# Kernel tuning notes

Hardware: AMD Instinct MI355X
Metric: run time of the kernel (lower is better)

Reference implementation:

```python
import jax, jax.numpy as jnp
import numpy as np

UNITS = 128
D_FEAT = 128
B, N = 4, 4096
EDGE_PROB = 0.01  # avg in-degree ~ N * EDGE_PROB ~ 41


def setup_inputs() -> dict:
    key = jax.random.key(0)
    k1, k2, k3, k4 = jax.random.split(key, 4)
    x = jax.random.normal(k1, (B, N, D_FEAT), dtype=jnp.float32)
    # binary adjacency mask, as consumed by tf.where(adj)
    adj = (jax.random.uniform(k2, (B, N, N)) < EDGE_PROB).astype(jnp.float32)
    # Dense(units, use_bias=False) kernels: msg on concat(x_snd, x_rec) -> [2d, U];
    # node_update on concat(x, messages) -> [d+U, U]
    W_msg = (jax.random.normal(k3, (2 * D_FEAT, UNITS), dtype=jnp.float32)
             / np.sqrt(2 * D_FEAT).astype(np.float32))
    W_upd = (jax.random.normal(k4, (D_FEAT + UNITS, UNITS), dtype=jnp.float32)
             / np.sqrt(D_FEAT + UNITS).astype(np.float32))
    return {"x": x, "adj": adj, "W_msg": W_msg, "W_upd": W_upd}


def reference(x, adj, W_msg, W_upd):
    # Faithful to MPNN2.call: edges are (b, s, r) where adj[b, s, r] != 0.
    # message per edge = concat(x[b,s], x[b,r]) @ W_msg = x[b,s]@Ws + x[b,r]@Wr.
    # messages[b,r] = segment_mean over incoming edges. Since the receiver term
    # x[b,r]@Wr is identical for all edges into r, its mean is itself, and the
    # sender term's mean is (adj^T @ (x@Ws)) / in_degree. Empty segments -> 0
    # (tf.math.unsorted_segment_mean semantics). This avoids data-dependent
    # edge-list shapes and is jit-compatible.
    d = x.shape[-1]
    Ws, Wr = W_msg[:d], W_msg[d:]          # [d, U] each
    xs = x @ Ws                            # sender contribution  [B, N, U]
    xr = x @ Wr                            # receiver contribution [B, N, U]
    deg = jnp.einsum('bsr->br', adj)[..., None]          # in-degree [B, N, 1]
    snd_sum = jnp.einsum('bsr,bsu->bru', adj, xs)        # [B, N, U]
    messages = jnp.where(deg > 0,
                         snd_sum / jnp.maximum(deg, 1.0) + xr,
                         0.0)
    # node_update on concat(x, messages); activation=None, use_bias=False
    return jnp.concatenate([x, messages], axis=-1) @ W_upd
```

## Files before the change

### kernel.cpp

```cpp
#include <hip/hip_runtime.h>
#include <hip/hip_bf16.h>

#define BB 4
#define NN 4096
#define ROWS (BB*NN)
#define RT 128
#define SC 512
#define NCH (NN/SC)
#define CAPC 32
#define BSTRIDE (NCH*CAPC)

typedef __attribute__((ext_vector_type(8))) short short8;
typedef __attribute__((ext_vector_type(4))) float f32x4;

__device__ __forceinline__ float asf(unsigned int u) {
    union { unsigned int i; float f; } cv; cv.i = u; return cv.f;
}
__device__ __forceinline__ unsigned short f2bf(float f) {
    union { float f; unsigned int i; } cv; cv.f = f;
    unsigned int i = cv.i;
    return (unsigned short)((i + 0x7FFFu + ((i >> 16) & 1u)) >> 16);
}

__global__ __launch_bounds__(256) void scan_bucket(const float* __restrict__ adj,
                                                   int* __restrict__ cnt2,
                                                   int* __restrict__ bucket) {
    __shared__ int lcnt[RT];
    int bI = blockIdx.x;
    int rt = bI & 31;
    int ch = (bI >> 5) & 7;
    int b  = bI >> 8;
    int r0 = rt * RT;
    int s0 = ch * SC;
    int t  = threadIdx.x;
    if (t < RT) lcnt[t] = 0;
    __syncthreads();
    int cg = t & 31;
    int sl = t >> 5;
    const float* base = adj + ((size_t)b * NN + s0) * NN + r0 + cg * 4;
    for (int k = 0; k < SC / 32; ++k) {
        float4 v[4];
#pragma unroll
        for (int u = 0; u < 4; ++u)
            v[u] = *(const float4*)(base + (size_t)(k * 32 + u * 8 + sl) * NN);
#pragma unroll
        for (int u = 0; u < 4; ++u) {
            int s = s0 + k * 32 + u * 8 + sl;
            float vals[4] = {v[u].x, v[u].y, v[u].z, v[u].w};
#pragma unroll
            for (int j = 0; j < 4; ++j) {
                if (vals[j] != 0.0f) {
                    int col = cg * 4 + j;
                    int slot = atomicAdd(&lcnt[col], 1);
                    if (slot < CAPC)
                        bucket[(size_t)((b << 12) + r0 + col) * BSTRIDE + ch * CAPC + slot] = s;
                }
            }
        }
    }
    __syncthreads();
    if (t < RT) cnt2[(size_t)((b << 12) + r0 + t) * NCH + ch] = lcnt[t];
}

__global__ __launch_bounds__(128) void fold_weights(const float* __restrict__ Wmsg,
                                                    const float* __restrict__ Wupd,
                                                    unsigned short* __restrict__ WcatT) {
    __shared__ float ldsS[128], ldsR[128];
    int k = blockIdx.x, t = threadIdx.x;
    ldsS[t] = Wmsg[k * 128 + t];
    ldsR[t] = Wmsg[(128 + k) * 128 + t];
    __syncthreads();
    float a1 = 0.f, a2 = 0.f;
#pragma unroll 8
    for (int m = 0; m < 128; ++m) {
        float wu = Wupd[(128 + m) * 128 + t];
        a1 += ldsS[m] * wu;
        a2 += ldsR[m] * wu;
    }
    WcatT[(size_t)t * 128 + k]         = f2bf(Wupd[k * 128 + t]);
    WcatT[(size_t)(128 + t) * 128 + k] = f2bf(a2);
    WcatT[(size_t)(256 + t) * 128 + k] = f2bf(a1);
}

__global__ __launch_bounds__(256) void gemm_mfma(const float* __restrict__ X,
                                                 const unsigned short* __restrict__ WcatT,
                                                 float* __restrict__ TD,
                                                 unsigned short* __restrict__ YB) {
    __shared__ unsigned short Al[64][136];
    __shared__ unsigned short Bl[128][136];
    int t  = threadIdx.x;
    int m0 = blockIdx.x * 64;
    int nb = blockIdx.y;

    {
        int m = t >> 2, seg = t & 3;
        const float* src = X + (size_t)(m0 + m) * 128 + seg * 32;
#pragma unroll
        for (int i = 0; i < 8; ++i) {
            float4 v = *(const float4*)(src + i * 4);
            ushort4 p;
            p.x = f2bf(v.x); p.y = f2bf(v.y); p.z = f2bf(v.z); p.w = f2bf(v.w);
            *(ushort4*)&Al[m][seg * 32 + i * 4] = p;
        }
    }
    {
        int n = t >> 1, half = t & 1;
        const unsigned short* src = WcatT + (size_t)(nb * 128 + n) * 128 + half * 64;
#pragma unroll
        for (int i = 0; i < 8; ++i) {
            uint4 v = *(const uint4*)(src + i * 8);
            *(uint4*)&Bl[n][half * 64 + i * 8] = v;
        }
    }
    __syncthreads();

    int lane = t & 63, wave = t >> 6;
    int quad = lane >> 4, lr = lane & 15;
    int wm = wave * 16;
    f32x4 acc[8];
#pragma unroll
    for (int s = 0; s < 8; ++s) acc[s] = (f32x4)0.f;

#pragma unroll
    for (int kk = 0; kk < 4; ++kk) {
        short8 a = *(short8*)&Al[wm + lr][kk * 32 + quad * 8];
#pragma unroll
        for (int s = 0; s < 8; ++s) {
            short8 bf = *(short8*)&Bl[s * 16 + lr][kk * 32 + quad * 8];
            acc[s] = __builtin_amdgcn_mfma_f32_16x16x32_bf16(a, bf, acc[s], 0, 0, 0);
        }
    }

    if (nb == 2) {
#pragma unroll
        for (int s = 0; s < 8; ++s)
#pragma unroll
            for (int r = 0; r < 4; ++r) {
                int row = m0 + wm + quad * 4 + r;
                YB[(size_t)row * 128 + s * 16 + lr] = f2bf(acc[s][r]);
            }
    } else {
#pragma unroll
        for (int s = 0; s < 8; ++s)
#pragma unroll
            for (int r = 0; r < 4; ++r) {
                int row = m0 + wm + quad * 4 + r;
                TD[(size_t)row * 256 + nb * 128 + s * 16 + lr] = acc[s][r];
            }
    }
}

__global__ __launch_bounds__(256) void gather_out(const float* __restrict__ TD,
                                                  const unsigned int* __restrict__ YB,
                                                  const int* __restrict__ cnt2,
                                                  const int* __restrict__ bucket,
                                                  float* __restrict__ out) {
    __shared__ int lds_s[4][BSTRIDE];
    int t  = threadIdx.x;
    int rs = t >> 6;
    int j2 = t & 63;
    int rg = blockIdx.x * 4 + rs;

    int c[NCH];
    int ctot = 0, deg = 0;
    int pre[NCH];
#pragma unroll
    for (int ch = 0; ch < NCH; ++ch) {
        c[ch] = cnt2[(size_t)rg * NCH + ch];
        deg += c[ch];
        int cc = min(c[ch], CAPC);
        pre[ch] = ctot;
        ctot += cc;
    }
#pragma unroll
    for (int ch = 0; ch < NCH; ++ch) {
        int cc = min(c[ch], CAPC);
        if (j2 < cc)
            lds_s[rs][pre[ch] + j2] = bucket[(size_t)rg * BSTRIDE + ch * CAPC + j2];
    }
    __syncthreads();

    const float2* td = (const float2*)(TD + (size_t)rg * 256);
    float2 t1 = td[j2];
    float2 res = t1;
    if (deg > 0) {
        int b = rg >> 12;
        const unsigned int* yb = YB + (((size_t)b << 12)) * 64 + j2;
        float al0 = 0.f, ah0 = 0.f, al1 = 0.f, ah1 = 0.f;
        float al2 = 0.f, ah2 = 0.f, al3 = 0.f, ah3 = 0.f;
        int e = 0;
        for (; e + 4 <= ctot; e += 4) {
            int s0 = lds_s[rs][e + 0];
            int s1 = lds_s[rs][e + 1];
            int s2 = lds_s[rs][e + 2];
            int s3 = lds_s[rs][e + 3];
            unsigned u0 = yb[(size_t)s0 * 64];
            unsigned u1 = yb[(size_t)s1 * 64];
            unsigned u2 = yb[(size_t)s2 * 64];
            unsigned u3 = yb[(size_t)s3 * 64];
            al0 += asf(u0 << 16); ah0 += asf(u0 & 0xffff0000u);
            al1 += asf(u1 << 16); ah1 += asf(u1 & 0xffff0000u);
            al2 += asf(u2 << 16); ah2 += asf(u2 & 0xffff0000u);
            al3 += asf(u3 << 16); ah3 += asf(u3 & 0xffff0000u);
        }
        for (; e < ctot; ++e) {
            unsigned u = yb[(size_t)lds_s[rs][e] * 64];
            al0 += asf(u << 16); ah0 += asf(u & 0xffff0000u);
        }
        float inv = 1.0f / (float)deg;
        float2 d2 = td[64 + j2];
        res.x = t1.x + d2.x + (al0 + al1 + al2 + al3) * inv;
        res.y = t1.y + d2.y + (ah0 + ah1 + ah2 + ah3) * inv;
    }
    ((float2*)(out + (size_t)rg * 128))[j2] = res;
}

extern "C" void kernel_launch(void* const* d_in, const int* in_sizes, int n_in,
                              void* d_out, int out_size, void* d_ws, size_t ws_size,
                              hipStream_t stream) {
    const float* x    = (const float*)d_in[0];
    const float* adj  = (const float*)d_in[1];
    const float* Wmsg = (const float*)d_in[2];
    const float* Wupd = (const float*)d_in[3];
    float* out = (float*)d_out;

    char* ws = (char*)d_ws;
    unsigned short* WcatT  = (unsigned short*)(ws);
    float*          TD     = (float*)(ws + 131072);
    unsigned short* YB     = (unsigned short*)(ws + 131072 + 16777216);
    int*            cnt2   = (int*)(ws + 131072 + 16777216 + 4194304);
    int*            bucket = (int*)(ws + 131072 + 16777216 + 4194304 + 524288);

    scan_bucket<<<1024, 256, 0, stream>>>(adj, cnt2, bucket);
    fold_weights<<<128, 128, 0, stream>>>(Wmsg, Wupd, WcatT);
    gemm_mfma<<<dim3(256, 3), 256, 0, stream>>>(x, WcatT, TD, YB);
    gather_out<<<ROWS / 4, 256, 0, stream>>>(TD, (const unsigned int*)YB, cnt2, bucket, out);
}
```

Measured before the change: 430.1 us.

## Scan full adjacency rows per block with double-buffered loads and finer sender chunks

The adjacency scan now has each block cover 32 full sender rows across all 4096 receivers, so reads are fully contiguous per row, and it double-buffers the row loads to overlap memory with atomic bucket insertion. Sender chunks shrink to 32 with capacity 8 per chunk, giving 128 chunks per receiver. The gather kernel rebuilds per-receiver edge lists with wave-level prefix scans over the 128 chunk counts. The risks are fewer blocks (512) for a bandwidth-bound scan, a larger count array, and strided reads of counts in the gather.

```diff
diff --git a/kernel.cpp b/kernel.cpp
--- a/kernel.cpp
+++ b/kernel.cpp
@@ -4,10 +4,9 @@
 #define BB 4
 #define NN 4096
 #define ROWS (BB*NN)
-#define RT 128
-#define SC 512
+#define SC 32
 #define NCH (NN/SC)
-#define CAPC 32
+#define CAPC 8
 #define BSTRIDE (NCH*CAPC)
 
 typedef __attribute__((ext_vector_type(8))) short short8;
@@ -25,41 +24,53 @@
 __global__ __launch_bounds__(256) void scan_bucket(const float* __restrict__ adj,
                                                    int* __restrict__ cnt2,
                                                    int* __restrict__ bucket) {
-    __shared__ int lcnt[RT];
-    int bI = blockIdx.x;
-    int rt = bI & 31;
-    int ch = (bI >> 5) & 7;
-    int b  = bI >> 8;
-    int r0 = rt * RT;
+    __shared__ int lcnt[NN];
+    int t  = threadIdx.x;
+    int ch = blockIdx.x & (NCH - 1);
+    int b  = blockIdx.x >> 7;
     int s0 = ch * SC;
-    int t  = threadIdx.x;
-    if (t < RT) lcnt[t] = 0;
-    __syncthreads();
-    int cg = t & 31;
-    int sl = t >> 5;
-    const float* base = adj + ((size_t)b * NN + s0) * NN + r0 + cg * 4;
-    for (int k = 0; k < SC / 32; ++k) {
-        float4 v[4];
-#pragma unroll
-        for (int u = 0; u < 4; ++u)
-            v[u] = *(const float4*)(base + (size_t)(k * 32 + u * 8 + sl) * NN);
-#pragma unroll
-        for (int u = 0; u < 4; ++u) {
-            int s = s0 + k * 32 + u * 8 + sl;
-            float vals[4] = {v[u].x, v[u].y, v[u].z, v[u].w};
+#pragma unroll
+    for (int i = 0; i < NN / 256; ++i) lcnt[i * 256 + t] = 0;
+    __syncthreads();
+
+    const float* base = adj + ((size_t)b * NN + s0) * NN;
+
+    float4 va[4], vb[4];
+    auto LOADROW = [&](float4* V, int r) {
+        const float4* rp = (const float4*)(base + (size_t)r * NN) + t;
+#pragma unroll
+        for (int i = 0; i < 4; ++i) V[i] = rp[i * 256];
+    };
+    auto PROCROW = [&](float4* V, int r) {
+        int s = s0 + r;
+#pragma unroll
+        for (int i = 0; i < 4; ++i) {
+            float vals[4] = {V[i].x, V[i].y, V[i].z, V[i].w};
 #pragma unroll
             for (int j = 0; j < 4; ++j) {
                 if (vals[j] != 0.0f) {
-                    int col = cg * 4 + j;
+                    int col = ((i << 8) + t) * 4 + j;
                     int slot = atomicAdd(&lcnt[col], 1);
                     if (slot < CAPC)
-                        bucket[(size_t)((b << 12) + r0 + col) * BSTRIDE + ch * CAPC + slot] = s;
+                        bucket[((size_t)((b << 12) + col) << 10) + (ch << 3) + slot] = s;
                 }
             }
         }
-    }
-    __syncthreads();
-    if (t < RT) cnt2[(size_t)((b << 12) + r0 + t) * NCH + ch] = lcnt[t];
+    };
+
+    LOADROW(va, 0);
+    for (int r = 0; r < SC; r += 2) {
+        LOADROW(vb, r + 1);
+        PROCROW(va, r);
+        if (r + 2 < SC) LOADROW(va, r + 2);
+        PROCROW(vb, r + 1);
+    }
+    __syncthreads();
+#pragma unroll
+    for (int i = 0; i < NN / 256; ++i) {
+        int col = i * 256 + t;
+        cnt2[((size_t)((b << 7) + ch) << 12) + col] = lcnt[col];
+    }
 }
 
 __global__ __launch_bounds__(128) void fold_weights(const float* __restrict__ Wmsg,
@@ -158,34 +169,42 @@
     __shared__ int lds_s[4][BSTRIDE];
     int t  = threadIdx.x;
     int rs = t >> 6;
-    int j2 = t & 63;
+    int l  = t & 63;
     int rg = blockIdx.x * 4 + rs;
-
-    int c[NCH];
-    int ctot = 0, deg = 0;
-    int pre[NCH];
-#pragma unroll
-    for (int ch = 0; ch < NCH; ++ch) {
-        c[ch] = cnt2[(size_t)rg * NCH + ch];
-        deg += c[ch];
-        int cc = min(c[ch], CAPC);
-        pre[ch] = ctot;
-        ctot += cc;
-    }
-#pragma unroll
-    for (int ch = 0; ch < NCH; ++ch) {
-        int cc = min(c[ch], CAPC);
-        if (j2 < cc)
-            lds_s[rs][pre[ch] + j2] = bucket[(size_t)rg * BSTRIDE + ch * CAPC + j2];
-    }
+    int b  = rg >> 12;
+    int r  = rg & (NN - 1);
+
+    int c0 = cnt2[((size_t)((b << 7) + l) << 12) + r];
+    int c1 = cnt2[((size_t)((b << 7) + 64 + l) << 12) + r];
+    int cc0 = min(c0, CAPC), cc1 = min(c1, CAPC);
+
+    int dsum = c0 + c1;
+#pragma unroll
+    for (int d = 32; d; d >>= 1) dsum += __shfl_xor(dsum, d, 64);
+    int deg = dsum;
+
+    int i0 = cc0;
+#pragma unroll
+    for (int d = 1; d < 64; d <<= 1) { int y = __shfl_up(i0, d, 64); if (l >= d) i0 += y; }
+    int i1 = cc1;
+#pragma unroll
+    for (int d = 1; d < 64; d <<= 1) { int y = __shfl_up(i1, d, 64); if (l >= d) i1 += y; }
+    int tot0 = __shfl(i0, 63, 64);
+    int tot1 = __shfl(i1, 63, 64);
+    int ex0  = i0 - cc0;
+    int ex1  = tot0 + i1 - cc1;
+    int ctot = tot0 + tot1;
+
+    const int* brow = bucket + ((size_t)rg << 10);
+    for (int k = 0; k < cc0; ++k) lds_s[rs][ex0 + k] = brow[(l << 3) + k];
+    for (int k = 0; k < cc1; ++k) lds_s[rs][ex1 + k] = brow[((64 + l) << 3) + k];
     __syncthreads();
 
     const float2* td = (const float2*)(TD + (size_t)rg * 256);
-    float2 t1 = td[j2];
+    float2 t1 = td[l];
     float2 res = t1;
     if (deg > 0) {
-        int b = rg >> 12;
-        const unsigned int* yb = YB + (((size_t)b << 12)) * 64 + j2;
+        const unsigned int* yb = YB + ((size_t)b << 12) * 64 + l;
         float al0 = 0.f, ah0 = 0.f, al1 = 0.f, ah1 = 0.f;
         float al2 = 0.f, ah2 = 0.f, al3 = 0.f, ah3 = 0.f;
         int e = 0;
@@ -208,11 +227,11 @@
             al0 += asf(u << 16); ah0 += asf(u & 0xffff0000u);
         }
         float inv = 1.0f / (float)deg;
-        float2 d2 = td[64 + j2];
+        float2 d2 = td[64 + l];
         res.x = t1.x + d2.x + (al0 + al1 + al2 + al3) * inv;
         res.y = t1.y + d2.y + (ah0 + ah1 + ah2 + ah3) * inv;
     }
-    ((float2*)(out + (size_t)rg * 128))[j2] = res;
+    ((float2*)(out + (size_t)rg * 128))[l] = res;
 }
 
 extern "C" void kernel_launch(void* const* d_in, const int* in_sizes, int n_in,
@@ -229,9 +248,9 @@
     float*          TD     = (float*)(ws + 131072);
     unsigned short* YB     = (unsigned short*)(ws + 131072 + 16777216);
     int*            cnt2   = (int*)(ws + 131072 + 16777216 + 4194304);
-    int*            bucket = (int*)(ws + 131072 + 16777216 + 4194304 + 524288);
-
-    scan_bucket<<<1024, 256, 0, stream>>>(adj, cnt2, bucket);
+    int*            bucket = (int*)(ws + 131072 + 16777216 + 4194304 + 8388608);
+
+    scan_bucket<<<BB * NCH, 256, 0, stream>>>(adj, cnt2, bucket);
     fold_weights<<<128, 128, 0, stream>>>(Wmsg, Wupd, WcatT);
     gemm_mfma<<<dim3(256, 3), 256, 0, stream>>>(x, WcatT, TD, YB);
     gather_out<<<ROWS / 4, 256, 0, stream>>>(TD, (const unsigned int*)YB, cnt2, bucket, out);
```

After: 456.1 us. +6.0%, slower.

## Replace bucket scan and gather with dense MFMA SpMM over adjacency

Applied to the files above, without the earlier changes.

Drops the sparse edge-bucketing scan and per-edge gather. Instead, a dense bf16 MFMA GEMM multiplies adj^T by a transposed bf16 YB, with the in-degree accumulated while loading each adjacency tile. The gemm epilogue now writes YB transposed per batch so the B operand reads are contiguous. This removes the CAPC=32 per-chunk cap that could truncate neighbours. The cost is dense compute over the whole 256MB adjacency, which becomes strided column loads, plus bf16 rounding of adjacency values (exact for 0/1).

```diff
diff --git a/kernel.cpp b/kernel.cpp
--- a/kernel.cpp
+++ b/kernel.cpp
@@ -1,65 +1,16 @@
 #include <hip/hip_runtime.h>
-#include <hip/hip_bf16.h>
 
 #define BB 4
 #define NN 4096
 #define ROWS (BB*NN)
-#define RT 128
-#define SC 512
-#define NCH (NN/SC)
-#define CAPC 32
-#define BSTRIDE (NCH*CAPC)
 
 typedef __attribute__((ext_vector_type(8))) short short8;
 typedef __attribute__((ext_vector_type(4))) float f32x4;
 
-__device__ __forceinline__ float asf(unsigned int u) {
-    union { unsigned int i; float f; } cv; cv.i = u; return cv.f;
-}
 __device__ __forceinline__ unsigned short f2bf(float f) {
     union { float f; unsigned int i; } cv; cv.f = f;
     unsigned int i = cv.i;
     return (unsigned short)((i + 0x7FFFu + ((i >> 16) & 1u)) >> 16);
-}
-
-__global__ __launch_bounds__(256) void scan_bucket(const float* __restrict__ adj,
-                                                   int* __restrict__ cnt2,
-                                                   int* __restrict__ bucket) {
-    __shared__ int lcnt[RT];
-    int bI = blockIdx.x;
-    int rt = bI & 31;
-    int ch = (bI >> 5) & 7;
-    int b  = bI >> 8;
-    int r0 = rt * RT;
-    int s0 = ch * SC;
-    int t  = threadIdx.x;
-    if (t < RT) lcnt[t] = 0;
-    __syncthreads();
-    int cg = t & 31;
-    int sl = t >> 5;
-    const float* base = adj + ((size_t)b * NN + s0) * NN + r0 + cg * 4;
-    for (int k = 0; k < SC / 32; ++k) {
-        float4 v[4];
-#pragma unroll
-        for (int u = 0; u < 4; ++u)
-            v[u] = *(const float4*)(base + (size_t)(k * 32 + u * 8 + sl) * NN);
-#pragma unroll
-        for (int u = 0; u < 4; ++u) {
-            int s = s0 + k * 32 + u * 8 + sl;
-            float vals[4] = {v[u].x, v[u].y, v[u].z, v[u].w};
-#pragma unroll
-            for (int j = 0; j < 4; ++j) {
-                if (vals[j] != 0.0f) {
-                    int col = cg * 4 + j;
-                    int slot = atomicAdd(&lcnt[col], 1);
-                    if (slot < CAPC)
-                        bucket[(size_t)((b << 12) + r0 + col) * BSTRIDE + ch * CAPC + slot] = s;
-                }
-            }
-        }
-    }
-    __syncthreads();
-    if (t < RT) cnt2[(size_t)((b << 12) + r0 + t) * NCH + ch] = lcnt[t];
 }
 
 __global__ __launch_bounds__(128) void fold_weights(const float* __restrict__ Wmsg,
@@ -85,7 +36,7 @@
 __global__ __launch_bounds__(256) void gemm_mfma(const float* __restrict__ X,
                                                  const unsigned short* __restrict__ WcatT,
                                                  float* __restrict__ TD,
-                                                 unsigned short* __restrict__ YB) {
+                                                 unsigned short* __restrict__ YBT) {
     __shared__ unsigned short Al[64][136];
     __shared__ unsigned short Bl[128][136];
     int t  = threadIdx.x;
@@ -132,13 +83,16 @@
     }
 
     if (nb == 2) {
-#pragma unroll
-        for (int s = 0; s < 8; ++s)
-#pragma unroll
-            for (int r = 0; r < 4; ++r) {
-                int row = m0 + wm + quad * 4 + r;
-                YB[(size_t)row * 128 + s * 16 + lr] = f2bf(acc[s][r]);
-            }
+        int b = m0 >> 12;
+        int s_base = (m0 & (NN - 1)) + wm + quad * 4;
+#pragma unroll
+        for (int s = 0; s < 8; ++s) {
+            int n = s * 16 + lr;
+            ushort4 p;
+            p.x = f2bf(acc[s][0]); p.y = f2bf(acc[s][1]);
+            p.z = f2bf(acc[s][2]); p.w = f2bf(acc[s][3]);
+            *(ushort4*)&YBT[(((size_t)(b << 7) + n) << 12) + s_base] = p;
+        }
     } else {
 #pragma unroll
         for (int s = 0; s < 8; ++s)
@@ -150,69 +104,100 @@
     }
 }
 
-__global__ __launch_bounds__(256) void gather_out(const float* __restrict__ TD,
-                                                  const unsigned int* __restrict__ YB,
-                                                  const int* __restrict__ cnt2,
-                                                  const int* __restrict__ bucket,
-                                                  float* __restrict__ out) {
-    __shared__ int lds_s[4][BSTRIDE];
+#define RT 32
+#define KT 128
+#define NT (NN/KT)
+__global__ __launch_bounds__(256) void spmm_out(const float* __restrict__ adj,
+                                                const unsigned short* __restrict__ YBT,
+                                                const float* __restrict__ TD,
+                                                float* __restrict__ out) {
+    __shared__ unsigned short At[RT][KT + 8];
+    __shared__ float degp[8][RT];
+    __shared__ float deg_s[RT];
+
     int t  = threadIdx.x;
-    int rs = t >> 6;
-    int j2 = t & 63;
-    int rg = blockIdx.x * 4 + rs;
-
-    int c[NCH];
-    int ctot = 0, deg = 0;
-    int pre[NCH];
-#pragma unroll
-    for (int ch = 0; ch < NCH; ++ch) {
-        c[ch] = cnt2[(size_t)rg * NCH + ch];
-        deg += c[ch];
-        int cc = min(c[ch], CAPC);
-        pre[ch] = ctot;
-        ctot += cc;
-    }
-#pragma unroll
-    for (int ch = 0; ch < NCH; ++ch) {
-        int cc = min(c[ch], CAPC);
-        if (j2 < cc)
-            lds_s[rs][pre[ch] + j2] = bucket[(size_t)rg * BSTRIDE + ch * CAPC + j2];
-    }
-    __syncthreads();
-
-    const float2* td = (const float2*)(TD + (size_t)rg * 256);
-    float2 t1 = td[j2];
-    float2 res = t1;
-    if (deg > 0) {
-        int b = rg >> 12;
-        const unsigned int* yb = YB + (((size_t)b << 12)) * 64 + j2;
-        float al0 = 0.f, ah0 = 0.f, al1 = 0.f, ah1 = 0.f;
-        float al2 = 0.f, ah2 = 0.f, al3 = 0.f, ah3 = 0.f;
-        int e = 0;
-        for (; e + 4 <= ctot; e += 4) {
-            int s0 = lds_s[rs][e + 0];
-            int s1 = lds_s[rs][e + 1];
-            int s2 = lds_s[rs][e + 2];
-            int s3 = lds_s[rs][e + 3];
-            unsigned u0 = yb[(size_t)s0 * 64];
-            unsigned u1 = yb[(size_t)s1 * 64];
-            unsigned u2 = yb[(size_t)s2 * 64];
-            unsigned u3 = yb[(size_t)s3 * 64];
-            al0 += asf(u0 << 16); ah0 += asf(u0 & 0xffff0000u);
-            al1 += asf(u1 << 16); ah1 += asf(u1 & 0xffff0000u);
-            al2 += asf(u2 << 16); ah2 += asf(u2 & 0xffff0000u);
-            al3 += asf(u3 << 16); ah3 += asf(u3 & 0xffff0000u);
-        }
-        for (; e < ctot; ++e) {
-            unsigned u = yb[(size_t)lds_s[rs][e] * 64];
-            al0 += asf(u << 16); ah0 += asf(u & 0xffff0000u);
-        }
-        float inv = 1.0f / (float)deg;
-        float2 d2 = td[64 + j2];
-        res.x = t1.x + d2.x + (al0 + al1 + al2 + al3) * inv;
-        res.y = t1.y + d2.y + (ah0 + ah1 + ah2 + ah3) * inv;
-    }
-    ((float2*)(out + (size_t)rg * 128))[j2] = res;
+    int r0 = blockIdx.x * RT;
+    int b  = blockIdx.y;
+    const float* adj_b = adj + (size_t)b * NN * NN;
+
+    int r  = t & 31;
+    int kg = t >> 5;
+    float va[16];
+    float dpart = 0.f;
+
+    int lane = t & 63, wave = t >> 6;
+    int wr = wave & 1, wn = wave >> 1;
+    int quad = lane >> 4, lr = lane & 15;
+    const unsigned short* ybt = YBT + ((size_t)b << 19);
+
+    f32x4 acc0 = (f32x4)0.f, acc1 = (f32x4)0.f, acc2 = (f32x4)0.f, acc3 = (f32x4)0.f;
+
+    {
+        const float* p = adj_b + (size_t)(kg * 16) * NN + r0 + r;
+#pragma unroll
+        for (int j = 0; j < 16; ++j) va[j] = p[(size_t)j * NN];
+    }
+
+    for (int tt = 0; tt < NT; ++tt) {
+        __syncthreads();
+        short8 w0, w1;
+#pragma unroll
+        for (int j = 0; j < 8; ++j) {
+            w0[j] = (short)f2bf(va[j]);
+            w1[j] = (short)f2bf(va[j + 8]);
+            dpart += va[j] + va[j + 8];
+        }
+        *(short8*)&At[r][kg * 16]     = w0;
+        *(short8*)&At[r][kg * 16 + 8] = w1;
+        __syncthreads();
+        if (tt + 1 < NT) {
+            const float* p = adj_b + (size_t)((tt + 1) * KT + kg * 16) * NN + r0 + r;
+#pragma unroll
+            for (int j = 0; j < 16; ++j) va[j] = p[(size_t)j * NN];
+        }
+        int k0 = tt * KT;
+#pragma unroll
+        for (int kk = 0; kk < 4; ++kk) {
+            short8 a = *(short8*)&At[wr * 16 + lr][kk * 32 + quad * 8];
+            const unsigned short* bp = ybt + (((size_t)(wn * 64 + lr)) << 12) + k0 + kk * 32 + quad * 8;
+            short8 b0 = *(const short8*)(bp);
+            short8 b1 = *(const short8*)(bp + (16 << 12));
+            short8 b2 = *(const short8*)(bp + (32 << 12));
+            short8 b3 = *(const short8*)(bp + (48 << 12));
+            acc0 = __builtin_amdgcn_mfma_f32_16x16x32_bf16(a, b0, acc0, 0, 0, 0);
+            acc1 = __builtin_amdgcn_mfma_f32_16x16x32_bf16(a, b1, acc1, 0, 0, 0);
+            acc2 = __builtin_amdgcn_mfma_f32_16x16x32_bf16(a, b2, acc2, 0, 0, 0);
+            acc3 = __builtin_amdgcn_mfma_f32_16x16x32_bf16(a, b3, acc3, 0, 0, 0);
+        }
+    }
+
+    __syncthreads();
+    degp[kg][r] = dpart;
+    __syncthreads();
+    if (t < RT) {
+        float s = 0.f;
+#pragma unroll
+        for (int g = 0; g < 8; ++g) s += degp[g][t];
+        deg_s[t] = s;
+    }
+    __syncthreads();
+
+    const float* td = TD + ((size_t)(b * NN + r0)) * 256;
+    float* ob = out + ((size_t)(b * NN + r0)) * 128;
+#pragma unroll
+    for (int sf = 0; sf < 4; ++sf) {
+        f32x4 a = (sf == 0) ? acc0 : (sf == 1) ? acc1 : (sf == 2) ? acc2 : acc3;
+        int n = wn * 64 + sf * 16 + lr;
+#pragma unroll
+        for (int rr = 0; rr < 4; ++rr) {
+            int rl = wr * 16 + quad * 4 + rr;
+            float deg = deg_s[rl];
+            float v = td[(size_t)rl * 256 + n];
+            if (deg > 0.f)
+                v += td[(size_t)rl * 256 + 128 + n] + a[rr] / deg;
+            ob[(size_t)rl * 128 + n] = v;
+        }
+    }
 }
 
 extern "C" void kernel_launch(void* const* d_in, const int* in_sizes, int n_in,
@@ -225,14 +210,11 @@
     float* out = (float*)d_out;
 
     char* ws = (char*)d_ws;
-    unsigned short* WcatT  = (unsigned short*)(ws);
-    float*          TD     = (float*)(ws + 131072);
-    unsigned short* YB     = (unsigned short*)(ws + 131072 + 16777216);
-    int*            cnt2   = (int*)(ws + 131072 + 16777216 + 4194304);
-    int*            bucket = (int*)(ws + 131072 + 16777216 + 4194304 + 524288);
-
-    scan_bucket<<<1024, 256, 0, stream>>>(adj, cnt2, bucket);
+    unsigned short* WcatT = (unsigned short*)(ws);
+    float*          TD    = (float*)(ws + 131072);
+    unsigned short* YBT   = (unsigned short*)(ws + 131072 + 16777216);
+
     fold_weights<<<128, 128, 0, stream>>>(Wmsg, Wupd, WcatT);
-    gemm_mfma<<<dim3(256, 3), 256, 0, stream>>>(x, WcatT, TD, YB);
-    gather_out<<<ROWS / 4, 256, 0, stream>>>(TD, (const unsigned int*)YB, cnt2, bucket, out);
-}
+    gemm_mfma<<<dim3(256, 3), 256, 0, stream>>>(x, WcatT, TD, YBT);
+    spmm_out<<<dim3(NN / RT, BB), 256, 0, stream>>>(adj, YBT, TD, out);
+}
```

Result: slower. 462.8 us (+7.6%).

## Compress adjacency to ballot bitmask and build per-receiver lists from bits

Applied to the files above, without the earlier changes.

The adjacency scan now emits a dense bitmask via wave ballots instead of per-receiver bucketed sender lists built with LDS atomics. Weight folding is merged into the scan kernel. The GEMM loads A directly from global into registers and reads B from global without LDS staging. The gather kernel rebuilds 16 receivers' sender lists per block from the bitmask before accumulating. This aims to cut scan overhead and launch count, but the gather now has to walk a full column of bits per block.

```diff
diff --git a/kernel.cpp b/kernel.cpp
--- a/kernel.cpp
+++ b/kernel.cpp
@@ -1,142 +1,120 @@
 #include <hip/hip_runtime.h>
-#include <hip/hip_bf16.h>
 
 #define BB 4
 #define NN 4096
-#define ROWS (BB*NN)
-#define RT 128
-#define SC 512
-#define NCH (NN/SC)
-#define CAPC 32
-#define BSTRIDE (NCH*CAPC)
 
 typedef __attribute__((ext_vector_type(8))) short short8;
 typedef __attribute__((ext_vector_type(4))) float f32x4;
 
-__device__ __forceinline__ float asf(unsigned int u) {
-    union { unsigned int i; float f; } cv; cv.i = u; return cv.f;
-}
 __device__ __forceinline__ unsigned short f2bf(float f) {
     union { float f; unsigned int i; } cv; cv.f = f;
     unsigned int i = cv.i;
     return (unsigned short)((i + 0x7FFFu + ((i >> 16) & 1u)) >> 16);
 }
-
-__global__ __launch_bounds__(256) void scan_bucket(const float* __restrict__ adj,
-                                                   int* __restrict__ cnt2,
-                                                   int* __restrict__ bucket) {
-    __shared__ int lcnt[RT];
-    int bI = blockIdx.x;
-    int rt = bI & 31;
-    int ch = (bI >> 5) & 7;
-    int b  = bI >> 8;
-    int r0 = rt * RT;
-    int s0 = ch * SC;
-    int t  = threadIdx.x;
-    if (t < RT) lcnt[t] = 0;
-    __syncthreads();
-    int cg = t & 31;
-    int sl = t >> 5;
-    const float* base = adj + ((size_t)b * NN + s0) * NN + r0 + cg * 4;
-    for (int k = 0; k < SC / 32; ++k) {
-        float4 v[4];
-#pragma unroll
-        for (int u = 0; u < 4; ++u)
-            v[u] = *(const float4*)(base + (size_t)(k * 32 + u * 8 + sl) * NN);
+__device__ __forceinline__ float asf(unsigned int u) {
+    union { unsigned int i; float f; } cv; cv.i = u; return cv.f;
+}
+
+__global__ __launch_bounds__(256) void kA(const float* __restrict__ adj,
+                                          const float* __restrict__ Wmsg,
+                                          const float* __restrict__ Wupd,
+                                          unsigned short* __restrict__ WcatT,
+                                          unsigned long long* __restrict__ bitT) {
+    __shared__ float fS[128], fR[128];
+    int bid = blockIdx.x, t = threadIdx.x;
+    if (bid < 128) {
+        int k = bid;
+        if (t < 128) { fS[t] = Wmsg[k * 128 + t]; fR[t] = Wmsg[(128 + k) * 128 + t]; }
+        __syncthreads();
+        if (t < 128) {
+            float a1 = 0.f, a2 = 0.f;
+#pragma unroll 8
+            for (int m = 0; m < 128; ++m) {
+                float wu = Wupd[(128 + m) * 128 + t];
+                a1 += fS[m] * wu;
+                a2 += fR[m] * wu;
+            }
+            WcatT[(size_t)t * 128 + k]         = f2bf(Wupd[k * 128 + t]);
+            WcatT[(size_t)(128 + t) * 128 + k] = f2bf(a2);
+            WcatT[(size_t)(256 + t) * 128 + k] = f2bf(a1);
+        }
+    }
+    int b  = bid >> 8;
+    int s0 = (bid & 255) * 16;
+    int wv = t >> 6, l = t & 63;
+    const float* ab = adj + ((size_t)b * NN + s0) * NN + wv * 1024 + l * 4;
+    unsigned long long* bt = bitT + ((size_t)(b * NN + s0) << 6);
+    for (int i = 0; i < 16; i += 4) {
+        float4 v0[4], v1[4], v2[4], v3[4];
+#pragma unroll
+        for (int it = 0; it < 4; ++it) {
+            v0[it] = *(const float4*)(ab + (size_t)(i + 0) * NN + it * 256);
+            v1[it] = *(const float4*)(ab + (size_t)(i + 1) * NN + it * 256);
+            v2[it] = *(const float4*)(ab + (size_t)(i + 2) * NN + it * 256);
+            v3[it] = *(const float4*)(ab + (size_t)(i + 3) * NN + it * 256);
+        }
 #pragma unroll
         for (int u = 0; u < 4; ++u) {
-            int s = s0 + k * 32 + u * 8 + sl;
-            float vals[4] = {v[u].x, v[u].y, v[u].z, v[u].w};
-#pragma unroll
-            for (int j = 0; j < 4; ++j) {
-                if (vals[j] != 0.0f) {
-                    int col = cg * 4 + j;
-                    int slot = atomicAdd(&lcnt[col], 1);
-                    if (slot < CAPC)
-                        bucket[(size_t)((b << 12) + r0 + col) * BSTRIDE + ch * CAPC + slot] = s;
+            float4* v = (u == 0) ? v0 : (u == 1) ? v1 : (u == 2) ? v2 : v3;
+            int row = i + u;
+#pragma unroll
+            for (int it = 0; it < 4; ++it) {
+                unsigned long long m0 = __ballot(v[it].x != 0.0f);
+                unsigned long long m1 = __ballot(v[it].y != 0.0f);
+                unsigned long long m2 = __ballot(v[it].z != 0.0f);
+                unsigned long long m3 = __ballot(v[it].w != 0.0f);
+                if (l < 4) {
+                    unsigned long long wd = (l == 0) ? m0 : (l == 1) ? m1 : (l == 2) ? m2 : m3;
+                    bt[((size_t)row << 6) + (wv * 4 + it) * 4 + l] = wd;
                 }
             }
         }
     }
-    __syncthreads();
-    if (t < RT) cnt2[(size_t)((b << 12) + r0 + t) * NCH + ch] = lcnt[t];
-}
-
-__global__ __launch_bounds__(128) void fold_weights(const float* __restrict__ Wmsg,
-                                                    const float* __restrict__ Wupd,
-                                                    unsigned short* __restrict__ WcatT) {
-    __shared__ float ldsS[128], ldsR[128];
-    int k = blockIdx.x, t = threadIdx.x;
-    ldsS[t] = Wmsg[k * 128 + t];
-    ldsR[t] = Wmsg[(128 + k) * 128 + t];
-    __syncthreads();
-    float a1 = 0.f, a2 = 0.f;
-#pragma unroll 8
-    for (int m = 0; m < 128; ++m) {
-        float wu = Wupd[(128 + m) * 128 + t];
-        a1 += ldsS[m] * wu;
-        a2 += ldsR[m] * wu;
-    }
-    WcatT[(size_t)t * 128 + k]         = f2bf(Wupd[k * 128 + t]);
-    WcatT[(size_t)(128 + t) * 128 + k] = f2bf(a2);
-    WcatT[(size_t)(256 + t) * 128 + k] = f2bf(a1);
-}
-
-__global__ __launch_bounds__(256) void gemm_mfma(const float* __restrict__ X,
-                                                 const unsigned short* __restrict__ WcatT,
-                                                 float* __restrict__ TD,
-                                                 unsigned short* __restrict__ YB) {
-    __shared__ unsigned short Al[64][136];
-    __shared__ unsigned short Bl[128][136];
-    int t  = threadIdx.x;
-    int m0 = blockIdx.x * 64;
-    int nb = blockIdx.y;
-
-    {
-        int m = t >> 2, seg = t & 3;
-        const float* src = X + (size_t)(m0 + m) * 128 + seg * 32;
-#pragma unroll
-        for (int i = 0; i < 8; ++i) {
-            float4 v = *(const float4*)(src + i * 4);
-            ushort4 p;
-            p.x = f2bf(v.x); p.y = f2bf(v.y); p.z = f2bf(v.z); p.w = f2bf(v.w);
-            *(ushort4*)&Al[m][seg * 32 + i * 4] = p;
-        }
-    }
-    {
-        int n = t >> 1, half = t & 1;
-        const unsigned short* src = WcatT + (size_t)(nb * 128 + n) * 128 + half * 64;
-#pragma unroll
-        for (int i = 0; i < 8; ++i) {
-            uint4 v = *(const uint4*)(src + i * 8);
-            *(uint4*)&Bl[n][half * 64 + i * 8] = v;
-        }
-    }
-    __syncthreads();
-
+}
+
+__global__ __launch_bounds__(256) void kB(const float* __restrict__ X,
+                                          const unsigned short* __restrict__ WcatT,
+                                          float* __restrict__ TD,
+                                          unsigned short* __restrict__ YB) {
+    int bid = blockIdx.x, t = threadIdx.x;
+    int m0 = (bid & 255) * 64;
+    int nb = bid >> 8;
     int lane = t & 63, wave = t >> 6;
     int quad = lane >> 4, lr = lane & 15;
-    int wm = wave * 16;
+    const float* xr = X + (size_t)(m0 + wave * 16 + lr) * 128;
+
+    auto LOADA = [&](int KK) -> short8 {
+        float4 f0 = *(const float4*)(xr + KK * 32 + quad * 8);
+        float4 f1 = *(const float4*)(xr + KK * 32 + quad * 8 + 4);
+        short8 av;
+        av[0] = (short)f2bf(f0.x); av[1] = (short)f2bf(f0.y);
+        av[2] = (short)f2bf(f0.z); av[3] = (short)f2bf(f0.w);
+        av[4] = (short)f2bf(f1.x); av[5] = (short)f2bf(f1.y);
+        av[6] = (short)f2bf(f1.z); av[7] = (short)f2bf(f1.w);
+        return av;
+    };
+    short8 a0 = LOADA(0), a1 = LOADA(1), a2 = LOADA(2), a3 = LOADA(3);
+
     f32x4 acc[8];
 #pragma unroll
     for (int s = 0; s < 8; ++s) acc[s] = (f32x4)0.f;
 
+    const unsigned short* wbase = WcatT + ((size_t)nb << 14) + (size_t)lr * 128 + quad * 8;
 #pragma unroll
     for (int kk = 0; kk < 4; ++kk) {
-        short8 a = *(short8*)&Al[wm + lr][kk * 32 + quad * 8];
+        short8 a = (kk == 0) ? a0 : (kk == 1) ? a1 : (kk == 2) ? a2 : a3;
 #pragma unroll
         for (int s = 0; s < 8; ++s) {
-            short8 bf = *(short8*)&Bl[s * 16 + lr][kk * 32 + quad * 8];
+            short8 bf = *(const short8*)(wbase + (size_t)(s * 16) * 128 + kk * 32);
             acc[s] = __builtin_amdgcn_mfma_f32_16x16x32_bf16(a, bf, acc[s], 0, 0, 0);
         }
     }
-
     if (nb == 2) {
 #pragma unroll
         for (int s = 0; s < 8; ++s)
 #pragma unroll
             for (int r = 0; r < 4; ++r) {
-                int row = m0 + wm + quad * 4 + r;
+                int row = m0 + wave * 16 + quad * 4 + r;
                 YB[(size_t)row * 128 + s * 16 + lr] = f2bf(acc[s][r]);
             }
     } else {
@@ -144,75 +122,79 @@
         for (int s = 0; s < 8; ++s)
 #pragma unroll
             for (int r = 0; r < 4; ++r) {
-                int row = m0 + wm + quad * 4 + r;
+                int row = m0 + wave * 16 + quad * 4 + r;
                 TD[(size_t)row * 256 + nb * 128 + s * 16 + lr] = acc[s][r];
             }
     }
 }
 
-__global__ __launch_bounds__(256) void gather_out(const float* __restrict__ TD,
-                                                  const unsigned int* __restrict__ YB,
-                                                  const int* __restrict__ cnt2,
-                                                  const int* __restrict__ bucket,
-                                                  float* __restrict__ out) {
-    __shared__ int lds_s[4][BSTRIDE];
-    int t  = threadIdx.x;
-    int rs = t >> 6;
-    int j2 = t & 63;
-    int rg = blockIdx.x * 4 + rs;
-
-    int c[NCH];
-    int ctot = 0, deg = 0;
-    int pre[NCH];
-#pragma unroll
-    for (int ch = 0; ch < NCH; ++ch) {
-        c[ch] = cnt2[(size_t)rg * NCH + ch];
-        deg += c[ch];
-        int cc = min(c[ch], CAPC);
-        pre[ch] = ctot;
-        ctot += cc;
-    }
-#pragma unroll
-    for (int ch = 0; ch < NCH; ++ch) {
-        int cc = min(c[ch], CAPC);
-        if (j2 < cc)
-            lds_s[rs][pre[ch] + j2] = bucket[(size_t)rg * BSTRIDE + ch * CAPC + j2];
-    }
+__global__ __launch_bounds__(256) void kC(const unsigned long long* __restrict__ bitT,
+                                          const unsigned int* __restrict__ YB32,
+                                          const float* __restrict__ TD,
+                                          float* __restrict__ out) {
+    __shared__ int cnt[16];
+    __shared__ unsigned short list[16][128];
+    int bid  = blockIdx.x, t = threadIdx.x;
+    int b    = bid >> 8;
+    int rg16 = bid & 255;
+    if (t < 16) cnt[t] = 0;
     __syncthreads();
 
-    const float2* td = (const float2*)(TD + (size_t)rg * 256);
-    float2 t1 = td[j2];
-    float2 res = t1;
-    if (deg > 0) {
-        int b = rg >> 12;
-        const unsigned int* yb = YB + (((size_t)b << 12)) * 64 + j2;
-        float al0 = 0.f, ah0 = 0.f, al1 = 0.f, ah1 = 0.f;
-        float al2 = 0.f, ah2 = 0.f, al3 = 0.f, ah3 = 0.f;
-        int e = 0;
-        for (; e + 4 <= ctot; e += 4) {
-            int s0 = lds_s[rs][e + 0];
-            int s1 = lds_s[rs][e + 1];
-            int s2 = lds_s[rs][e + 2];
-            int s3 = lds_s[rs][e + 3];
-            unsigned u0 = yb[(size_t)s0 * 64];
-            unsigned u1 = yb[(size_t)s1 * 64];
-            unsigned u2 = yb[(size_t)s2 * 64];
-            unsigned u3 = yb[(size_t)s3 * 64];
-            al0 += asf(u0 << 16); ah0 += asf(u0 & 0xffff0000u);
-            al1 += asf(u1 << 16); ah1 += asf(u1 & 0xffff0000u);
-            al2 += asf(u2 << 16); ah2 += asf(u2 & 0xffff0000u);
-            al3 += asf(u3 << 16); ah3 += asf(u3 & 0xffff0000u);
-        }
-        for (; e < ctot; ++e) {
-            unsigned u = yb[(size_t)lds_s[rs][e] * 64];
-            al0 += asf(u << 16); ah0 += asf(u & 0xffff0000u);
-        }
-        float inv = 1.0f / (float)deg;
-        float2 d2 = td[64 + j2];
-        res.x = t1.x + d2.x + (al0 + al1 + al2 + al3) * inv;
-        res.y = t1.y + d2.y + (ah0 + ah1 + ah2 + ah3) * inv;
-    }
-    ((float2*)(out + (size_t)rg * 128))[j2] = res;
+    int g  = rg16 >> 4;
+    int l0 = (rg16 & 15) * 4;
+    const unsigned long long* bt = bitT + ((size_t)(b * NN) << 6) + (g << 2);
+    for (int i = 0; i < NN / 256; ++i) {
+        int s = t + 256 * i;
+        const unsigned long long* p = bt + ((size_t)s << 6);
+        unsigned long long w0 = p[0], w1 = p[1], w2 = p[2], w3 = p[3];
+        unsigned n0 = (unsigned)(w0 >> l0) & 0xFu;
+        unsigned n1 = (unsigned)(w1 >> l0) & 0xFu;
+        unsigned n2 = (unsigned)(w2 >> l0) & 0xFu;
+        unsigned n3 = (unsigned)(w3 >> l0) & 0xFu;
+        while (n0) { int i2 = __ffs(n0) - 1; n0 &= n0 - 1; int c = 4 * i2;     int sl = atomicAdd(&cnt[c], 1); if (sl < 128) list[c][sl] = (unsigned short)s; }
+        while (n1) { int i2 = __ffs(n1) - 1; n1 &= n1 - 1; int c = 4 * i2 + 1; int sl = atomicAdd(&cnt[c], 1); if (sl < 128) list[c][sl] = (unsigned short)s; }
+        while (n2) { int i2 = __ffs(n2) - 1; n2 &= n2 - 1; int c = 4 * i2 + 2; int sl = atomicAdd(&cnt[c], 1); if (sl < 128) list[c][sl] = (unsigned short)s; }
+        while (n3) { int i2 = __ffs(n3) - 1; n3 &= n3 - 1; int c = 4 * i2 + 3; int sl = atomicAdd(&cnt[c], 1); if (sl < 128) list[c][sl] = (unsigned short)s; }
+    }
+    __syncthreads();
+
+    int lane = t & 63, w = t >> 6;
+    const unsigned int* yb = YB32 + ((size_t)b << 18) + lane;
+    for (int q = 0; q < 4; ++q) {
+        int c   = w * 4 + q;
+        int rgl = b * NN + rg16 * 16 + c;
+        int deg = cnt[c];
+        int ctot = min(deg, 128);
+        const float2* td = (const float2*)(TD + (size_t)rgl * 256);
+        float2 t1 = td[lane];
+        float2 res = t1;
+        if (deg > 0) {
+            float al0 = 0.f, ah0 = 0.f, al1 = 0.f, ah1 = 0.f;
+            float al2 = 0.f, ah2 = 0.f, al3 = 0.f, ah3 = 0.f;
+            const unsigned short* ls = list[c];
+            int e = 0;
+            for (; e + 4 <= ctot; e += 4) {
+                int s0 = ls[e], s1 = ls[e + 1], s2 = ls[e + 2], s3 = ls[e + 3];
+                unsigned u0 = yb[(size_t)s0 << 6];
+                unsigned u1 = yb[(size_t)s1 << 6];
+                unsigned u2 = yb[(size_t)s2 << 6];
+                unsigned u3 = yb[(size_t)s3 << 6];
+                al0 += asf(u0 << 16); ah0 += asf(u0 & 0xffff0000u);
+                al1 += asf(u1 << 16); ah1 += asf(u1 & 0xffff0000u);
+                al2 += asf(u2 << 16); ah2 += asf(u2 & 0xffff0000u);
+                al3 += asf(u3 << 16); ah3 += asf(u3 & 0xffff0000u);
+            }
+            for (; e < ctot; ++e) {
+                unsigned u = yb[(size_t)ls[e] << 6];
+                al0 += asf(u << 16); ah0 += asf(u & 0xffff0000u);
+            }
+            float inv = 1.0f / (float)deg;
+            float2 d2 = td[64 + lane];
+            res.x = t1.x + d2.x + (al0 + al1 + al2 + al3) * inv;
+            res.y = t1.y + d2.y + (ah0 + ah1 + ah2 + ah3) * inv;
+        }
+        ((float2*)(out + (size_t)rgl * 128))[lane] = res;
+    }
 }
 
 extern "C" void kernel_launch(void* const* d_in, const int* in_sizes, int n_in,
@@ -225,14 +207,12 @@
     float* out = (float*)d_out;
 
     char* ws = (char*)d_ws;
-    unsigned short* WcatT  = (unsigned short*)(ws);
-    float*          TD     = (float*)(ws + 131072);
-    unsigned short* YB     = (unsigned short*)(ws + 131072 + 16777216);
-    int*            cnt2   = (int*)(ws + 131072 + 16777216 + 4194304);
-    int*            bucket = (int*)(ws + 131072 + 16777216 + 4194304 + 524288);
-
-    scan_bucket<<<1024, 256, 0, stream>>>(adj, cnt2, bucket);
-    fold_weights<<<128, 128, 0, stream>>>(Wmsg, Wupd, WcatT);
-    gemm_mfma<<<dim3(256, 3), 256, 0, stream>>>(x, WcatT, TD, YB);
-    gather_out<<<ROWS / 4, 256, 0, stream>>>(TD, (const unsigned int*)YB, cnt2, bucket, out);
-}
+    unsigned short*     WcatT = (unsigned short*)(ws);
+    float*              TD    = (float*)(ws + 131072);
+    unsigned short*     YB    = (unsigned short*)(ws + 131072 + 16777216);
+    unsigned long long* bitT  = (unsigned long long*)(ws + 131072 + 16777216 + 4194304);
+
+    kA<<<1024, 256, 0, stream>>>(adj, Wmsg, Wupd, WcatT, bitT);
+    kB<<<768, 256, 0, stream>>>(x, WcatT, TD, YB);
+    kC<<<1024, 256, 0, stream>>>(bitT, (const unsigned int*)YB, TD, out);
+}
```

Result: no change. 430.3 us (+0.0%).
